# Kernel optimization log

Measured on AMD Instinct MI355X. Metric: run time of the kernel, lower is better.

Reference implementation:

```python
import jax, jax.numpy as jnp
import numpy as np

B, T, D = 4, 2048, 2048
K, D_B, TOPK, WINDOW = 7, 128, 16, 64
GATE_CAP = 1.0
STRAND_CAP = 1.0
_PHI = 1.618033988749895
_PSI = -0.6180339887498949


def _ln(x, g, b, eps=1e-5):
    m = jnp.mean(x, axis=-1, keepdims=True)
    v = jnp.mean((x - m) ** 2, axis=-1, keepdims=True)
    return (x - m) * jax.lax.rsqrt(v + eps) * g + b


def setup_inputs() -> dict:
    ks = jax.random.split(jax.random.key(0), 20)
    rn = lambda k, s, sc=1.0: jax.random.normal(k, s, jnp.float32) * sc
    d_s = 1.0 / np.sqrt(D)
    db_s = 1.0 / np.sqrt(D_B)
    return {
        'X_write': rn(ks[0], (B, T, D)),
        'X_read': rn(ks[1], (B, T, D)),
        'slots': rn(ks[2], (B, K, D_B)),
        'W0': rn(ks[3], (D, D), d_s),
        'ln_write_g': jnp.ones((D,), jnp.float32),
        'ln_write_b': jnp.zeros((D,), jnp.float32),
        'Wv': rn(ks[4], (D_B, D), d_s),
        'Wk': rn(ks[5], (D_B, D_B), db_s),
        'slot_key_bias': rn(ks[6], (K, D_B), 2.0),
        'Wg_w': rn(ks[7], (D_B, 2 * D_B), 1.0 / np.sqrt(2 * D_B)),
        'Wg_b': jnp.full((D_B,), -2.0, jnp.float32),
        'ln_strand_g': jnp.ones((D_B,), jnp.float32),
        'ln_strand_b': jnp.zeros((D_B,), jnp.float32),
        'Wsq': rn(ks[8], (D_B, D_B), db_s),
        'Wsk': rn(ks[9], (D_B, D_B), db_s),
        'Wsv': rn(ks[10], (D_B, D_B), db_s),
        'lambda_strand': rn(ks[11], (D_B,), 0.1),
        'Wq_read': rn(ks[12], (D_B, D), d_s),
        'Wk_read': rn(ks[13], (D_B, D_B), db_s),
        'Wv_read': rn(ks[14], (D, D_B), db_s),
        'render_coeffs': rn(ks[15], (K, 3, D), 0.1),
        'slot_temps': 1.0 + rn(ks[16], (K,), 0.1),
    }


def reference(X_write, X_read, slots, W0, ln_write_g, ln_write_b, Wv, Wk,
              slot_key_bias, Wg_w, Wg_b, ln_strand_g, ln_strand_b,
              Wsq, Wsk, Wsv, lambda_strand, Wq_read, Wk_read, Wv_read,
              render_coeffs, slot_temps):
    b, t, d = X_write.shape
    sd = 1.0 / np.sqrt(D_B)
    X_n = _ln(X_write, ln_write_g, ln_write_b)

    # --- banded salience + topk (torch.no_grad region; only int indices escape) ---
    W_eff = min(WINDOW, t - 1)
    Xs = jax.lax.stop_gradient(X_n)
    X_W0 = Xs @ jax.lax.stop_gradient(W0).T            # [b,t,d]
    Xp = jnp.pad(X_W0, ((0, 0), (W_eff, 0), (0, 0)))   # left-pad so offset w -> j = i + w - W

    def band_dot(w):
        return jnp.einsum('btd,btd->bt', Xs,
                          jax.lax.dynamic_slice_in_dim(Xp, w, t, axis=1))

    band = jax.vmap(band_dot)(jnp.arange(W_eff)).transpose(1, 2, 0)  # [b,t,W]
    ii = jnp.arange(t)[:, None]
    ww = jnp.arange(W_eff)[None, :]
    jj = ii + ww - W_eff
    valid = (jj >= 0) & (ii >= 1)                      # j in [max(0,i-W), i)
    sal = jnp.where(valid, band, -jnp.inf).reshape(b, -1)
    topk_eff = min(TOPK, t * (t - 1) // 2)
    _, idx = jax.lax.top_k(sal, topk_eff)              # [b,topk]
    i_idx = idx // W_eff
    j_idx = i_idx + (idx % W_eff) - W_eff

    # --- topk pair gather + bilinear relation ---
    x_new = jnp.take_along_axis(X_n, i_idx[..., None], axis=1)  # [b,topk,d]
    x_old = jnp.take_along_axis(X_n, j_idx[..., None], axis=1)
    pair_sal = jnp.sum(x_new * (x_old @ jax.lax.stop_gradient(W0).T), axis=-1)
    alpha = jax.nn.softmax(pair_sal, axis=-1)
    R_t = jnp.einsum('bp,bpe->be', alpha, (x_new - x_old) @ Wv.T)  # [b,d_b]

    # --- slot write ---
    slot_keys = slots @ Wk.T + slot_key_bias[None]
    compat = jnp.einsum('bke,be->bk', slot_keys, R_t) * sd
    compat = compat * jax.nn.softplus(slot_temps)[None]
    sw = jax.nn.softmax(compat, axis=-1)
    weighted_R = sw[..., None] * R_t[:, None, :]                 # [b,K,d_b]
    g = jax.nn.sigmoid(jnp.concatenate([slots, weighted_R], -1) @ Wg_w.T + Wg_b)
    slots_upd = (1.0 - g) * slots + g * weighted_R

    # --- strand mixer (KxK self-attention) ---
    B_ln = _ln(slots_upd, ln_strand_g, ln_strand_b)
    att = jax.nn.softmax(jnp.einsum('bke,bme->bkm', B_ln @ Wsq.T, B_ln @ Wsk.T) * sd, axis=-1)
    ctx = att @ (B_ln @ Wsv.T)
    slots_next = slots_upd + ctx * jnp.clip(jnp.tanh(lambda_strand), -STRAND_CAP, STRAND_CAP)

    # --- aux losses ---
    L_persist = jnp.mean((slots_next - slots) ** 2)
    nrm = jnp.linalg.norm(slots_next, axis=-1, keepdims=True)
    Bn = slots_next / jnp.maximum(nrm, 1e-12)
    cos = jnp.einsum('bke,bme->bkm', Bn, Bn)
    off = 1.0 - jnp.eye(K, dtype=cos.dtype)
    L_div = jnp.sum(cos ** 2 * off) / (b * K * (K - 1))

    # --- directional render gate + read ---
    q_r = X_read @ Wq_read.T                    # [b,t,d_b]
    k_r = slots_next @ Wk_read.T                # [b,K,d_b]
    v_r = slots_next @ Wv_read.T                # [b,K,d]
    scores = jnp.einsum('bte,bke->btk', q_r, k_r) * sd
    q_mean = jnp.mean(X_read, axis=1)           # [b,d]
    w0q = q_mean @ jax.lax.stop_gradient(W0).T
    dphi = _PHI - _PSI
    phi_q = (w0q - _PSI * q_mean) / dphi
    psi_q = (_PHI * q_mean - w0q) / dphi
    pm = jnp.linalg.norm(phi_q, axis=-1, keepdims=True)
    sm = jnp.linalg.norm(psi_q, axis=-1, keepdims=True)
    tot = pm + sm + 1e-6
    basis = jnp.concatenate([jnp.ones_like(pm), pm / tot, sm / tot], axis=-1)  # [b,3]
    gate = jnp.clip(jnp.tanh(jnp.einsum('bi,kid->bkd', basis, render_coeffs)),
                    -GATE_CAP, GATE_CAP)
    z = jnp.einsum('btk,bkd->btd', jax.nn.softmax(scores, axis=-1), v_r * gate)
    return z, slots_next, L_persist, L_div
```

## Files before the change

### kernel.cpp

```cpp
#include <hip/hip_runtime.h>
#include <cstdint>
#include <cstddef>

#define DEV __device__ __forceinline__

typedef __bf16 bf16x8 __attribute__((ext_vector_type(8)));
typedef float f32x4 __attribute__((ext_vector_type(4)));
typedef unsigned short u16;
typedef unsigned int u32;

constexpr int Bq = 4, Tq = 2048, Dq = 2048, Kq = 7, DB = 128, TK = 16;
constexpr float SD = 0.08838834764831845f;
constexpr float PHIc = 1.618033988749895f;
constexpr float PSIc = -0.6180339887498949f;
constexpr float DPHI = 2.2360679774997896f;
#define NEG_INF (-__builtin_inff())

DEV u16 f2bf(float f) {
  union { float f; u32 u; } x; x.f = f;
  u32 r = (x.u + 0x7fffu + ((x.u >> 16) & 1u)) >> 16;
  return (u16)r;
}
DEV float bfbits2f(u32 h) { union { u32 u; float f; } x; x.u = h << 16; return x.f; }

DEV void async16(void* l, const void* g) {
  __builtin_amdgcn_global_load_lds((const __attribute__((address_space(1))) void*)g,
                                   (__attribute__((address_space(3))) void*)l, 16, 0, 0);
}

__global__ __launch_bounds__(256) void k_prep(const float* __restrict__ W0, u16* __restrict__ W0b,
                                              const float* __restrict__ Xw, const float* __restrict__ g,
                                              const float* __restrict__ bb, u16* __restrict__ Xn,
                                              const float* __restrict__ Xr, float* __restrict__ part) {
  int bid = blockIdx.x;
  int tid = threadIdx.x;
  if (bid < 2048) {
    size_t i = ((size_t)bid * 256 + tid) * 8;
    float4 a = *(const float4*)&W0[i];
    float4 c = *(const float4*)&W0[i + 4];
    u32 p0 = (u32)f2bf(a.x) | ((u32)f2bf(a.y) << 16);
    u32 p1 = (u32)f2bf(a.z) | ((u32)f2bf(a.w) << 16);
    u32 p2 = (u32)f2bf(c.x) | ((u32)f2bf(c.y) << 16);
    u32 p3 = (u32)f2bf(c.z) | ((u32)f2bf(c.w) << 16);
    uint4 st; st.x = p0; st.y = p1; st.z = p2; st.w = p3;
    *(uint4*)&W0b[i] = st;
  } else if (bid < 2048 + 8192) {
    int row = bid - 2048;
    const float* xr = Xw + (size_t)row * Dq;
    int lane = tid & 63, w = tid >> 6;
    float4 a = *(const float4*)&xr[tid * 8];
    float4 c = *(const float4*)&xr[tid * 8 + 4];
    float s = a.x + a.y + a.z + a.w + c.x + c.y + c.z + c.w;
    float q = a.x*a.x + a.y*a.y + a.z*a.z + a.w*a.w + c.x*c.x + c.y*c.y + c.z*c.z + c.w*c.w;
    #pragma unroll
    for (int o = 32; o; o >>= 1) { s += __shfl_xor(s, o); q += __shfl_xor(q, o); }
    __shared__ float red[8];
    if (lane == 0) { red[w] = s; red[w + 4] = q; }
    __syncthreads();
    float S = red[0] + red[1] + red[2] + red[3];
    float Q = red[4] + red[5] + red[6] + red[7];
    float mean = S * (1.0f / Dq);
    float var = Q * (1.0f / Dq) - mean * mean;
    float rstd = rsqrtf(var + 1e-5f);
    float v[8] = {a.x, a.y, a.z, a.w, c.x, c.y, c.z, c.w};
    u32 p[4];
    #pragma unroll
    for (int j = 0; j < 4; ++j) {
      int d0 = tid * 8 + j * 2;
      float o0 = (v[j*2]   - mean) * rstd * g[d0]   + bb[d0];
      float o1 = (v[j*2+1] - mean) * rstd * g[d0+1] + bb[d0+1];
      p[j] = (u32)f2bf(o0) | ((u32)f2bf(o1) << 16);
    }
    uint4 st; st.x = p[0]; st.y = p[1]; st.z = p[2]; st.w = p[3];
    *(uint4*)&Xn[(size_t)row * Dq + tid * 8] = st;
  } else {
    int f = bid - (2048 + 8192);
    int s = f & 1, y = (f >> 1) & 31, b = f >> 6;
    const float* xb = Xr + (size_t)b * Tq * Dq + (size_t)s * 1024 + tid * 4;
    f32x4 acc = {0.f, 0.f, 0.f, 0.f};
    #pragma unroll 4
    for (int t = 0; t < 64; ++t) {
      const float4 v = *(const float4*)&xb[(size_t)(y * 64 + t) * Dq];
      acc[0] += v.x; acc[1] += v.y; acc[2] += v.z; acc[3] += v.w;
    }
    float4 st; st.x = acc[0]; st.y = acc[1]; st.z = acc[2]; st.w = acc[3];
    *(float4*)&part[((size_t)(b * 32 + y)) * Dq + s * 1024 + tid * 4] = st;
  }
}

__global__ __launch_bounds__(256) void k_gemm(const u16* __restrict__ A, const u16* __restrict__ B,
                                              u16* __restrict__ C, int M, int N, int K,
                                              const float* __restrict__ part, float* __restrict__ qm) {
  __shared__ u16 As[128 * 64], Bs[128 * 64];
  int tid = threadIdx.x;
  if (blockIdx.y == 16) {
    int bm = blockIdx.x;
    if (bm >= 8) return;
    int s = bm & 1, b = bm >> 1;
    int col = s * 1024 + tid * 4;
    f32x4 acc = {0.f, 0.f, 0.f, 0.f};
    #pragma unroll 8
    for (int y = 0; y < 32; ++y) {
      float4 v = *(const float4*)&part[((size_t)(b * 32 + y)) * Dq + col];
      acc[0] += v.x; acc[1] += v.y; acc[2] += v.z; acc[3] += v.w;
    }
    float4 st;
    st.x = acc[0] * (1.0f / Tq); st.y = acc[1] * (1.0f / Tq);
    st.z = acc[2] * (1.0f / Tq); st.w = acc[3] * (1.0f / Tq);
    *(float4*)&qm[(size_t)b * Dq + col] = st;
    return;
  }
  int lane = tid & 63, w = tid >> 6, wr = w >> 1, wc = w & 1;
  int bm = blockIdx.x, bn = blockIdx.y;
  const u16* Ab = A + (size_t)bm * 128 * K;
  const u16* Bb = B + (size_t)bn * 128 * K;
  f32x4 zero = {0.f, 0.f, 0.f, 0.f};
  f32x4 acc[4][4];
  #pragma unroll
  for (int mi = 0; mi < 4; ++mi)
    #pragma unroll
    for (int ni = 0; ni < 4; ++ni) acc[mi][ni] = zero;
  int ro = tid >> 3;
  int co = (tid & 7) * 8;
  int cs = co ^ ((ro & 7) * 8);
  for (int k0 = 0; k0 < K; k0 += 64) {
    #pragma unroll
    for (int i = 0; i < 4; ++i) {
      int row = ro + i * 32;
      async16(&As[row * 64 + co], Ab + (size_t)row * K + k0 + cs);
      async16(&Bs[row * 64 + co], Bb + (size_t)row * K + k0 + cs);
    }
    __syncthreads();
    #pragma unroll
    for (int ks = 0; ks < 2; ++ks) {
      int cbase = ks * 32 + ((lane >> 4) * 8);
      int crd = cbase ^ ((lane & 7) * 8);
      bf16x8 af[4], bfr[4];
      #pragma unroll
      for (int mi = 0; mi < 4; ++mi)
        af[mi] = *(const bf16x8*)&As[(wr * 64 + mi * 16 + (lane & 15)) * 64 + crd];
      #pragma unroll
      for (int ni = 0; ni < 4; ++ni)
        bfr[ni] = *(const bf16x8*)&Bs[(wc * 64 + ni * 16 + (lane & 15)) * 64 + crd];
      #pragma unroll
      for (int mi = 0; mi < 4; ++mi)
        #pragma unroll
        for (int ni = 0; ni < 4; ++ni)
          acc[mi][ni] = __builtin_amdgcn_mfma_f32_16x16x32_bf16(af[mi], bfr[ni], acc[mi][ni], 0, 0, 0);
    }
    __syncthreads();
  }
  int r0 = bm * 128 + wr * 64, c0 = bn * 128 + wc * 64;
  #pragma unroll
  for (int mi = 0; mi < 4; ++mi)
    #pragma unroll
    for (int ni = 0; ni < 4; ++ni) {
      int col = c0 + ni * 16 + (lane & 15);
      int rb = r0 + mi * 16 + ((lane >> 4) * 4);
      #pragma unroll
      for (int rg = 0; rg < 4; ++rg)
        C[(size_t)(rb + rg) * N + col] = f2bf(acc[mi][ni][rg]);
    }
}

__global__ __launch_bounds__(768) void k_band(const u16* __restrict__ Xn, const u16* __restrict__ XW0,
                                              float* __restrict__ sal,
                                              const float* __restrict__ W0, const float* __restrict__ qm,
                                              float* __restrict__ w0q) {
  int tid = threadIdx.x, lane = tid & 63, w = tid >> 6;
  if (blockIdx.y == Bq) {
    int x = blockIdx.x;
    for (int r = w; r < 32; r += 12) {
      int d = x * 32 + r;
      const float* wr = W0 + (size_t)d * Dq;
      float a0 = 0, a1 = 0, a2 = 0, a3 = 0;
      for (int e = lane * 4; e < Dq; e += 256) {
        float4 wv = *(const float4*)&wr[e];
        float4 q0 = *(const float4*)&qm[0 * Dq + e];
        float4 q1 = *(const float4*)&qm[1 * Dq + e];
        float4 q2 = *(const float4*)&qm[2 * Dq + e];
        float4 q3 = *(const float4*)&qm[3 * Dq + e];
        a0 += wv.x*q0.x + wv.y*q0.y + wv.z*q0.z + wv.w*q0.w;
        a1 += wv.x*q1.x + wv.y*q1.y + wv.z*q1.z + wv.w*q1.w;
        a2 += wv.x*q2.x + wv.y*q2.y + wv.z*q2.z + wv.w*q2.w;
        a3 += wv.x*q3.x + wv.y*q3.y + wv.z*q3.z + wv.w*q3.w;
      }
      #pragma unroll
      for (int o = 32; o; o >>= 1) {
        a0 += __shfl_xor(a0, o); a1 += __shfl_xor(a1, o);
        a2 += __shfl_xor(a2, o); a3 += __shfl_xor(a3, o);
      }
      if (lane == 0) {
        w0q[0 * Dq + d] = a0; w0q[1 * Dq + d] = a1;
        w0q[2 * Dq + d] = a2; w0q[3 * Dq + d] = a3;
      }
    }
    return;
  }
  int b = blockIdx.y, i0 = blockIdx.x * 32;
  int mi = w / 6, ni = w % 6;
  const u16* Xb = Xn + (size_t)b * Tq * Dq;
  const u16* Wb = XW0 + (size_t)b * Tq * Dq;
  int koff = (lane >> 4) * 8;
  const u16* ap = Xb + (size_t)(i0 + mi * 16 + (lane & 15)) * Dq + koff;
  int j = i0 - 64 + ni * 16 + (lane & 15); j = min(max(j, 0), Tq - 1);
  const u16* bp = Wb + (size_t)j * Dq + koff;
  f32x4 zero = {0.f, 0.f, 0.f, 0.f};
  f32x4 accA = zero, accB = zero;
  for (int k = 0; k < Dq; k += 64) {
    bf16x8 a0 = *(const bf16x8*)(ap + k);
    bf16x8 b0 = *(const bf16x8*)(bp + k);
    bf16x8 a1 = *(const bf16x8*)(ap + k + 32);
    bf16x8 b1 = *(const bf16x8*)(bp + k + 32);
    accA = __builtin_amdgcn_mfma_f32_16x16x32_bf16(a0, b0, accA, 0, 0, 0);
    accB = __builtin_amdgcn_mfma_f32_16x16x32_bf16(a1, b1, accB, 0, 0, 0);
  }
  int nl = ni * 16 + (lane & 15);
  #pragma unroll
  for (int rg = 0; rg < 4; ++rg) {
    int i = i0 + mi * 16 + (lane >> 4) * 4 + rg;
    int wb = nl - (i - i0);
    if (wb >= 0 && wb < 64) {
      int jj = i0 - 64 + nl;
      bool valid = (jj >= 0) && (i >= 1);
      sal[((size_t)b * Tq + i) * 64 + wb] = valid ? (accA[rg] + accB[rg]) : NEG_INF;
    }
  }
}

__global__ __launch_bounds__(256) void k_topk1(const float* __restrict__ sal,
                                               float* __restrict__ cv, int* __restrict__ ci,
                                               const float* __restrict__ qm, const float* __restrict__ w0q,
                                               float* __restrict__ basis) {
  int b = blockIdx.y, tid = threadIdx.x, lane = tid & 63;
  if (blockIdx.x == 128) {
    __shared__ float red[256];
    __shared__ float psum;
    float ps = 0, ss = 0;
    for (int d = tid; d < Dq; d += 256) {
      float qv = qm[b * Dq + d], wv = w0q[b * Dq + d];
      float ph = (wv - PSIc * qv) * (1.0f / DPHI);
      float pv = (PHIc * qv - wv) * (1.0f / DPHI);
      ps += ph * ph; ss += pv * pv;
    }
    red[tid] = ps; __syncthreads();
    for (int st = 128; st; st >>= 1) { if (tid < st) red[tid] += red[tid + st]; __syncthreads(); }
    if (tid == 0) psum = red[0];
    __syncthreads();
    red[tid] = ss; __syncthreads();
    for (int st = 128; st; st >>= 1) { if (tid < st) red[tid] += red[tid + st]; __syncthreads(); }
    if (tid == 0) {
      float pm = sqrtf(psum), sm = sqrtf(red[0]);
      float tot = pm + sm + 1e-6f;
      basis[b * 3 + 0] = 1.0f; basis[b * 3 + 1] = pm / tot; basis[b * 3 + 2] = sm / tot;
    }
    return;
  }
  int chunk = blockIdx.x;
  const float* s = sal + (size_t)b * Tq * 64 + (size_t)chunk * 1024;
  float lv[4]; int li[4];
  #pragma unroll
  for (int i = 0; i < 4; ++i) { lv[i] = NEG_INF; li[i] = -1; }
  #pragma unroll
  for (int i = 0; i < 4; ++i) {
    int e = tid + i * 256;
    float v = s[e];
    int idx = chunk * 1024 + e;
    if (v > lv[3]) {
      lv[3] = v; li[3] = idx;
      #pragma unroll
      for (int q = 3; q > 0; --q)
        if (lv[q] > lv[q - 1]) {
          float tv = lv[q]; lv[q] = lv[q - 1]; lv[q - 1] = tv;
          int t2 = li[q]; li[q] = li[q - 1]; li[q - 1] = t2;
        }
    }
  }
  __shared__ float Sv[256][4];
  __shared__ int Si[256][4];
  __shared__ int heads[256];
  #pragma unroll
  for (int i = 0; i < 4; ++i) { Sv[tid][i] = lv[i]; Si[tid][i] = li[i]; }
  heads[tid] = 0;
  __syncthreads();
  float* ov = cv + ((size_t)b * 128 + chunk) * 16;
  int* oi = ci + ((size_t)b * 128 + chunk) * 16;
  for (int r = 0; r < 16; ++r) {
    if (tid < 64) {
      float best = NEG_INF; int bl = 0; int bidx = 0x7fffffff;
      #pragma unroll
      for (int cc = 0; cc < 4; ++cc) {
        int c = lane + cc * 64;
        int h = heads[c];
        float v = (h < 4) ? Sv[c][h] : NEG_INF;
        int ix = (h < 4) ? Si[c][h] : 0x7fffffff;
        if (v > best || (v == best && ix < bidx)) { best = v; bl = c; bidx = ix; }
      }
      #pragma unroll
      for (int o = 32; o; o >>= 1) {
        float bv = __shfl_xor(best, o); int blx = __shfl_xor(bl, o); int bix = __shfl_xor(bidx, o);
        if (bv > best || (bv == best && bix < bidx)) { best = bv; bl = blx; bidx = bix; }
      }
      if (lane == 0) {
        int h = heads[bl];
        ov[r] = best; oi[r] = (h < 4) ? Si[bl][h] : -1;
        heads[bl] = h + 1;
      }
    }
    __syncthreads();
  }
}

__global__ __launch_bounds__(256) void k_topk2(const float* __restrict__ cv, const int* __restrict__ ci,
                                               int* __restrict__ ti, int* __restrict__ tj) {
  int b = blockIdx.x, tid = threadIdx.x, lane = tid & 63;
  __shared__ float Sv[128][16];
  __shared__ int Si[128][16];
  __shared__ int heads[128];
  __shared__ int ridx[16];
  for (int i = tid; i < 128 * 16; i += 256) {
    ((float*)Sv)[i] = cv[(size_t)b * 2048 + i];
    ((int*)Si)[i] = ci[(size_t)b * 2048 + i];
  }
  if (tid < 128) heads[tid] = 0;
  __syncthreads();
  for (int r = 0; r < 16; ++r) {
    if (tid < 64) {
      float best = NEG_INF; int bl = 0; int bidx = 0x7fffffff;
      #pragma unroll
      for (int cc = 0; cc < 2; ++cc) {
        int c = lane + cc * 64;
        int h = heads[c];
        float v = (h < 16) ? Sv[c][h] : NEG_INF;
        int ix = (h < 16) ? Si[c][h] : 0x7fffffff;
        if (v > best || (v == best && ix < bidx)) { best = v; bl = c; bidx = ix; }
      }
      #pragma unroll
      for (int o = 32; o; o >>= 1) {
        float bv = __shfl_xor(best, o); int blx = __shfl_xor(bl, o); int bix = __shfl_xor(bidx, o);
        if (bv > best || (bv == best && bix < bidx)) { best = bv; bl = blx; bidx = bix; }
      }
      if (lane == 0) {
        int h = heads[bl];
        ridx[r] = Si[bl][h];
        heads[bl] = h + 1;
      }
    }
    __syncthreads();
  }
  if (tid < 16) {
    int fi = ridx[tid];
    int ii = fi >> 6;
    int jj = ii + (fi & 63) - 64;
    ti[b * TK + tid] = ii;
    tj[b * TK + tid] = jj;
  }
}

__global__ __launch_bounds__(256) void k_gatherln(const float* __restrict__ X, const float* __restrict__ g,
    const float* __restrict__ bb, const int* __restrict__ ti, const int* __restrict__ tj,
    float* __restrict__ Xnew, float* __restrict__ Xold, float* __restrict__ psal) {
  int b = blockIdx.y, p = blockIdx.x >> 1, side = blockIdx.x & 1;
  int tid = threadIdx.x, lane = tid & 63, w = tid >> 6;
  if (blockIdx.x == 0 && tid < TK) psal[b * TK + tid] = 0.f;
  int row = side ? tj[b * TK + p] : ti[b * TK + p];
  row = min(max(row, 0), Tq - 1);
  const float* xr = X + ((size_t)(b * Tq + row)) * Dq;
  float* dst = (side ? Xold : Xnew) + ((size_t)(b * TK + p)) * Dq;
  float4 a = *(const float4*)&xr[tid * 8];
  float4 c = *(const float4*)&xr[tid * 8 + 4];
  float s = a.x + a.y + a.z + a.w + c.x + c.y + c.z + c.w;
  float q = a.x*a.x + a.y*a.y + a.z*a.z + a.w*a.w + c.x*c.x + c.y*c.y + c.z*c.z + c.w*c.w;
  #pragma unroll
  for (int o = 32; o; o >>= 1) { s += __shfl_xor(s, o); q += __shfl_xor(q, o); }
  __shared__ float red[8];
  if (lane == 0) { red[w] = s; red[w + 4] = q; }
  __syncthreads();
  float S = red[0] + red[1] + red[2] + red[3];
  float Q = red[4] + red[5] + red[6] + red[7];
  float mean = S * (1.0f / Dq);
  float var = Q * (1.0f / Dq) - mean * mean;
  float rstd = rsqrtf(var + 1e-5f);
  float v[8] = {a.x, a.y, a.z, a.w, c.x, c.y, c.z, c.w};
  float o8[8];
  #pragma unroll
  for (int j = 0; j < 8; ++j) {
    int d = tid * 8 + j;
    o8[j] = (v[j] - mean) * rstd * g[d] + bb[d];
  }
  float4 s0; s0.x = o8[0]; s0.y = o8[1]; s0.z = o8[2]; s0.w = o8[3];
  float4 s1; s1.x = o8[4]; s1.y = o8[5]; s1.z = o8[6]; s1.w = o8[7];
  *(float4*)&dst[tid * 8] = s0;
  *(float4*)&dst[tid * 8 + 4] = s1;
}

__global__ __launch_bounds__(256) void k_pairsal(const float* __restrict__ W0, const float* __restrict__ Xnew,
                                                 const float* __restrict__ Xold, float* __restrict__ psal) {
  int d0 = blockIdx.x * 64, e0 = blockIdx.y * 64;
  int tid = threadIdx.x, P = tid & 63, dg = tid >> 6;
  f32x4 xo[16];
  #pragma unroll
  for (int i = 0; i < 16; ++i)
    xo[i] = *(const f32x4*)&Xold[(size_t)P * Dq + e0 + i * 4];
  int dbase = d0 + dg * 16;
  f32x4 xn[4];
  #pragma unroll
  for (int i = 0; i < 4; ++i)
    xn[i] = *(const f32x4*)&Xnew[(size_t)P * Dq + dbase + i * 4];
  float acc = 0.f;
  #pragma unroll
  for (int dd = 0; dd < 16; ++dd) {
    int d = __builtin_amdgcn_readfirstlane(dbase + dd);
    const float* wr = W0 + (size_t)d * Dq + e0;
    float i0 = 0.f, i1 = 0.f, i2 = 0.f, i3 = 0.f;
    #pragma unroll
    for (int i = 0; i < 16; ++i) {
      float4 wv = *(const float4*)&wr[i * 4];
      i0 += wv.x * xo[i][0]; i1 += wv.y * xo[i][1];
      i2 += wv.z * xo[i][2]; i3 += wv.w * xo[i][3];
    }
    acc += xn[dd >> 2][dd & 3] * ((i0 + i1) + (i2 + i3));
  }
  __shared__ float part[4][64];
  part[dg][P] = acc;
  __syncthreads();
  if (tid < 64)
    atomicAdd(&psal[tid], part[0][tid] + part[1][tid] + part[2][tid] + part[3][tid]);
}

__global__ __launch_bounds__(256) void k_alphart(const float* __restrict__ psal, const float* __restrict__ Xnew,
    const float* __restrict__ Xold, const float* __restrict__ Wv, float* __restrict__ Rt) {
  int bx = blockIdx.x, b = blockIdx.y;
  int tid = threadIdx.x, lane = tid & 63, w = tid >> 6;
  __shared__ float al[16], xd[Dq];
  if (tid == 0) {
    float mx = NEG_INF;
    #pragma unroll
    for (int p = 0; p < 16; ++p) mx = fmaxf(mx, psal[b * 16 + p]);
    float ee[16]; float s = 0.f;
    #pragma unroll
    for (int p = 0; p < 16; ++p) { ee[p] = expf(psal[b * 16 + p] - mx); s += ee[p]; }
    #pragma unroll
    for (int p = 0; p < 16; ++p) al[p] = ee[p] / s;
  }
  __syncthreads();
  {
    int d0 = tid * 8;
    float a8[8] = {0, 0, 0, 0, 0, 0, 0, 0};
    #pragma unroll
    for (int p = 0; p < 16; ++p) {
      const float* xn = Xnew + (size_t)(b * 16 + p) * Dq + d0;
      const float* xo = Xold + (size_t)(b * 16 + p) * Dq + d0;
      float ap = al[p];
      float4 n0 = *(const float4*)xn;
      float4 n1 = *(const float4*)(xn + 4);
      float4 o0 = *(const float4*)xo;
      float4 o1 = *(const float4*)(xo + 4);
      a8[0] += ap * (n0.x - o0.x); a8[1] += ap * (n0.y - o0.y);
      a8[2] += ap * (n0.z - o0.z); a8[3] += ap * (n0.w - o0.w);
      a8[4] += ap * (n1.x - o1.x); a8[5] += ap * (n1.y - o1.y);
      a8[6] += ap * (n1.z - o1.z); a8[7] += ap * (n1.w - o1.w);
    }
    #pragma unroll
    for (int j = 0; j < 8; ++j) xd[d0 + j] = a8[j];
  }
  __syncthreads();
  int e = bx * 4 + w;
  const float* wr = Wv + (size_t)e * Dq;
  float s = 0.f;
  #pragma unroll 8
  for (int d = lane; d < Dq; d += 64) s += wr[d] * xd[d];
  #pragma unroll
  for (int o = 32; o; o >>= 1) s += __shfl_xor(s, o);
  if (lane == 0) Rt[b * DB + e] = s;
}

__global__ __launch_bounds__(256) void ksl_a(const float* __restrict__ slots, const float* __restrict__ Wk,
    const float* __restrict__ skb, const float* __restrict__ Rt, const float* __restrict__ temps,
    float* __restrict__ compat) {
  int k = blockIdx.x, b = blockIdx.y;
  int tid = threadIdx.x, g = tid >> 4, sub = tid & 15;
  __shared__ float s_s[DB], r_s[DB], sk_s[DB];
  if (tid < DB) { s_s[tid] = slots[((size_t)(b * Kq + k)) * DB + tid]; r_s[tid] = Rt[b * DB + tid]; }
  __syncthreads();
  #pragma unroll
  for (int r = 0; r < 8; ++r) {
    int e = g * 8 + r;
    const float* wr = Wk + e * DB;
    float a = 0.f;
    #pragma unroll
    for (int j = 0; j < 8; ++j) a += wr[sub + j * 16] * s_s[sub + j * 16];
    a += __shfl_xor(a, 8); a += __shfl_xor(a, 4); a += __shfl_xor(a, 2); a += __shfl_xor(a, 1);
    if (sub == 0) sk_s[e] = a + skb[k * DB + e];
  }
  __syncthreads();
  if (tid < 64) {
    float a = sk_s[tid] * r_s[tid] + sk_s[tid + 64] * r_s[tid + 64];
    #pragma unroll
    for (int o = 32; o; o >>= 1) a += __shfl_xor(a, o);
    if (tid == 0) {
      float t = temps[k];
      compat[b * Kq + k] = a * SD * log1pf(expf(t));
    }
  }
}

__global__ __launch_bounds__(256) void ksl_c(const float* __restrict__ slots, const float* __restrict__ Rt,
    const float* __restrict__ compat, const float* __restrict__ Wgw, const float* __restrict__ Wgb,
    const float* __restrict__ lng, const float* __restrict__ lnb,
    const float* __restrict__ Wsq, const float* __restrict__ Wsk, const float* __restrict__ Wsv,
    float* __restrict__ suOut, float* __restrict__ qqOut, float* __restrict__ kkOut,
    float* __restrict__ vvOut) {
  int k = blockIdx.x, b = blockIdx.y;
  int tid = threadIdx.x, g = tid >> 4, sub = tid & 15;
  __shared__ float s_s[DB], r_s[DB], su[DB], bnl[DB];
  __shared__ float mvm, mvr;
  if (tid < DB) { s_s[tid] = slots[((size_t)(b * Kq + k)) * DB + tid]; r_s[tid] = Rt[b * DB + tid]; }
  __syncthreads();
  float swk;
  {
    float cm[Kq]; float mx = NEG_INF;
    #pragma unroll
    for (int kk = 0; kk < Kq; ++kk) { cm[kk] = compat[b * Kq + kk]; mx = fmaxf(mx, cm[kk]); }
    float ssum = 0.f;
    #pragma unroll
    for (int kk = 0; kk < Kq; ++kk) { cm[kk] = expf(cm[kk] - mx); ssum += cm[kk]; }
    swk = cm[k] / ssum;
  }
  #pragma unroll
  for (int r = 0; r < 8; ++r) {
    int e = g * 8 + r;
    const float* wr = Wgw + e * 256;
    float a = 0.f;
    #pragma unroll
    for (int j = 0; j < 16; ++j) {
      int col = sub + j * 16;
      float x = (j < 8) ? s_s[col] : swk * r_s[col - 128];
      a += wr[col] * x;
    }
    a += __shfl_xor(a, 8); a += __shfl_xor(a, 4); a += __shfl_xor(a, 2); a += __shfl_xor(a, 1);
    if (sub == 0) {
      a += Wgb[e];
      float gv = 1.0f / (1.0f + expf(-a));
      float wrv = swk * r_s[e];
      su[e] = (1.0f - gv) * s_s[e] + gv * wrv;
    }
  }
  __syncthreads();
  if (tid < 64) {
    float v0 = su[tid], v1 = su[tid + 64];
    float s = v0 + v1, q = v0 * v0 + v1 * v1;
    #pragma unroll
    for (int o = 32; o; o >>= 1) { s += __shfl_xor(s, o); q += __shfl_xor(q, o); }
    if (tid == 0) {
      float m = s / DB; float va = q / DB - m * m;
      mvm = m; mvr = rsqrtf(va + 1e-5f);
    }
  }
  __syncthreads();
  if (tid < DB) {
    bnl[tid] = (su[tid] - mvm) * mvr * lng[tid] + lnb[tid];
    suOut[((size_t)(b * Kq + k)) * DB + tid] = su[tid];
  }
  __syncthreads();
  #pragma unroll
  for (int r = 0; r < 8; ++r) {
    int e = g * 8 + r;
    const float* wr1 = Wsq + e * DB;
    const float* wr2 = Wsk + e * DB;
    const float* wr3 = Wsv + e * DB;
    float a1 = 0.f, a2 = 0.f, a3 = 0.f;
    #pragma unroll
    for (int j = 0; j < 8; ++j) {
      float x = bnl[sub + j * 16];
      a1 += wr1[sub + j * 16] * x;
      a2 += wr2[sub + j * 16] * x;
      a3 += wr3[sub + j * 16] * x;
    }
    #pragma unroll
    for (int o = 8; o; o >>= 1) {
      a1 += __shfl_xor(a1, o); a2 += __shfl_xor(a2, o); a3 += __shfl_xor(a3, o);
    }
    if (sub == 0) {
      size_t oi = ((size_t)(b * Kq + k)) * DB + e;
      qqOut[oi] = a1; kkOut[oi] = a2; vvOut[oi] = a3;
    }
  }
}

__global__ __launch_bounds__(256) void ksl_d(const float* __restrict__ suOut, const float* __restrict__ qqOut,
    const float* __restrict__ kkOut, const float* __restrict__ vvOut, const float* __restrict__ lam,
    const float* __restrict__ Wkr, float* __restrict__ snOut, float* __restrict__ krOut) {
  int k = blockIdx.x, b = blockIdx.y;
  int tid = threadIdx.x, g = tid >> 4, sub = tid & 15;
  __shared__ float qq[DB], kks[Kq][DB], vvs[Kq][DB], att[8], sn_s[DB];
  if (tid < DB) qq[tid] = qqOut[((size_t)(b * Kq + k)) * DB + tid];
  for (int i = tid; i < Kq * DB; i += 256) {
    ((float*)kks)[i] = kkOut[(size_t)b * Kq * DB + i];
    ((float*)vvs)[i] = vvOut[(size_t)b * Kq * DB + i];
  }
  __syncthreads();
  if (tid < 112) {
    int m = g;
    float a = 0.f;
    #pragma unroll
    for (int j = 0; j < 8; ++j) a += qq[sub + j * 16] * kks[m][sub + j * 16];
    a += __shfl_xor(a, 8); a += __shfl_xor(a, 4); a += __shfl_xor(a, 2); a += __shfl_xor(a, 1);
    if (sub == 0) att[m] = a * SD;
  }
  __syncthreads();
  if (tid == 0) {
    float mx = att[0];
    for (int m = 1; m < Kq; ++m) mx = fmaxf(mx, att[m]);
    float s = 0.f;
    for (int m = 0; m < Kq; ++m) { att[m] = expf(att[m] - mx); s += att[m]; }
    for (int m = 0; m < Kq; ++m) att[m] /= s;
  }
  __syncthreads();
  if (tid < DB) {
    float c = 0.f;
    #pragma unroll
    for (int m = 0; m < Kq; ++m) c += att[m] * vvs[m][tid];
    float l = tanhf(lam[tid]); l = fminf(fmaxf(l, -1.0f), 1.0f);
    float v = suOut[((size_t)(b * Kq + k)) * DB + tid] + c * l;
    sn_s[tid] = v;
    snOut[((size_t)(b * Kq + k)) * DB + tid] = v;
  }
  __syncthreads();
  #pragma unroll
  for (int r = 0; r < 8; ++r) {
    int e = g * 8 + r;
    const float* wr = Wkr + e * DB;
    float a = 0.f;
    #pragma unroll
    for (int j = 0; j < 8; ++j) a += wr[sub + j * 16] * sn_s[sub + j * 16];
    a += __shfl_xor(a, 8); a += __shfl_xor(a, 4); a += __shfl_xor(a, 2); a += __shfl_xor(a, 1);
    if (sub == 0) krOut[((size_t)(b * Kq + k)) * DB + e] = a;
  }
}

__global__ __launch_bounds__(256) void k_mvg(const float* __restrict__ snOut, const float* __restrict__ krOut,
    const float* __restrict__ Wqr, const float* __restrict__ Wvr, const float* __restrict__ rc,
    const float* __restrict__ basis, const float* __restrict__ slots,
    u16* __restrict__ Mb, u16* __restrict__ Vgb, float* __restrict__ out2) {
  int b = blockIdx.y, tid = threadIdx.x;
  if (blockIdx.x == 8) {
    if (b != 0) return;
    __shared__ float red[256];
    __shared__ float nrm[28];
    float p = 0.f;
    for (int i = tid; i < Bq * Kq * DB; i += 256) { float d = snOut[i] - slots[i]; p += d * d; }
    red[tid] = p; __syncthreads();
    for (int st = 128; st; st >>= 1) { if (tid < st) red[tid] += red[tid + st]; __syncthreads(); }
    if (tid == 0) out2[0] = red[0] / (float)(Bq * Kq * DB);
    if (tid < 28) {
      int bb2 = tid / 7, k = tid % 7;
      float s = 0.f;
      for (int e = 0; e < DB; ++e) { float v = snOut[(size_t)(bb2 * 7 + k) * DB + e]; s += v * v; }
      nrm[tid] = fmaxf(sqrtf(s), 1e-12f);
    }
    __syncthreads();
    float dv = 0.f;
    if (tid < 168) {
      int bb2 = tid / 42, r = tid % 42;
      int k = r / 6, m = r % 6; m += (m >= k);
      float dot = 0.f;
      for (int e = 0; e < DB; ++e)
        dot += snOut[(size_t)(bb2 * 7 + k) * DB + e] * snOut[(size_t)(bb2 * 7 + m) * DB + e];
      float c = dot / (nrm[bb2 * 7 + k] * nrm[bb2 * 7 + m]);
      dv = c * c;
    }
    red[tid] = dv; __syncthreads();
    for (int st = 128; st; st >>= 1) { if (tid < st) red[tid] += red[tid + st]; __syncthreads(); }
    if (tid == 0) out2[1] = red[0] / 168.0f;
    return;
  }
  int d = blockIdx.x * 256 + tid;
  __shared__ float krs[Kq][DB], sns[Kq][DB];
  for (int i = tid; i < Kq * DB; i += 256) {
    ((float*)krs)[i] = krOut[(size_t)b * Kq * DB + i];
    ((float*)sns)[i] = snOut[(size_t)b * Kq * DB + i];
  }
  __syncthreads();
  float b0 = basis[b * 3 + 0], b1 = basis[b * 3 + 1], b2 = basis[b * 3 + 2];
  float am[7] = {0, 0, 0, 0, 0, 0, 0};
  for (int e = 0; e < DB; ++e) {
    float wq = Wqr[(size_t)e * Dq + d];
    #pragma unroll
    for (int k = 0; k < 7; ++k) am[k] += krs[k][e] * wq;
  }
  float vr[7] = {0, 0, 0, 0, 0, 0, 0};
  const float* wvrow = Wvr + (size_t)d * DB;
  for (int e = 0; e < DB; ++e) {
    float wv = wvrow[e];
    #pragma unroll
    for (int k = 0; k < 7; ++k) vr[k] += sns[k][e] * wv;
  }
  #pragma unroll
  for (int k = 0; k < 7; ++k) {
    Mb[((size_t)b * 7 + k) * Dq + d] = f2bf(am[k]);
    float gt = tanhf(b0 * rc[((size_t)k * 3 + 0) * Dq + d] +
                     b1 * rc[((size_t)k * 3 + 1) * Dq + d] +
                     b2 * rc[((size_t)k * 3 + 2) * Dq + d]);
    gt = fminf(fmaxf(gt, -1.0f), 1.0f);
    Vgb[((size_t)b * 7 + k) * Dq + d] = f2bf(vr[k] * gt);
  }
}

__global__ __launch_bounds__(256) void k_z(const float* __restrict__ X, const u16* __restrict__ Mb,
                                           const u16* __restrict__ Vgb, float* __restrict__ Z) {
  int b = blockIdx.y, t0 = blockIdx.x * 16;
  int tid = threadIdx.x, lane = tid & 63, w = tid >> 6;
  const u16* Ms = Mb + (size_t)b * 7 * 2048;
  const u16* Vs = Vgb + (size_t)b * 7 * 2048;
  for (int ri = 0; ri < 4; ++ri) {
    int t = t0 + ri * 4 + w;
    const float* xr = X + ((size_t)b * Tq + t) * Dq;
    float sc[7] = {0, 0, 0, 0, 0, 0, 0};
    #pragma unroll
    for (int i = 0; i < 8; ++i) {
      int d = lane * 4 + i * 256;
      float4 x = *(const float4*)&xr[d];
      #pragma unroll
      for (int k = 0; k < 7; ++k) {
        uint2 mm = *(const uint2*)&Ms[k * 2048 + d];
        sc[k] += x.x * bfbits2f(mm.x & 0xffffu) + x.y * bfbits2f(mm.x >> 16)
               + x.z * bfbits2f(mm.y & 0xffffu) + x.w * bfbits2f(mm.y >> 16);
      }
    }
    #pragma unroll
    for (int k = 0; k < 7; ++k) {
      #pragma unroll
      for (int o = 32; o; o >>= 1) sc[k] += __shfl_xor(sc[k], o);
    }
    float mx = sc[0];
    #pragma unroll
    for (int k = 1; k < 7; ++k) mx = fmaxf(mx, sc[k]);
    float pz[7]; float s = 0.f;
    #pragma unroll
    for (int k = 0; k < 7; ++k) { pz[k] = expf((sc[k] - mx) * SD); s += pz[k]; }
    float inv = 1.0f / s;
    #pragma unroll
    for (int k = 0; k < 7; ++k) pz[k] *= inv;
    float* zr = Z + ((size_t)b * Tq + t) * Dq;
    #pragma unroll
    for (int i = 0; i < 8; ++i) {
      int d = lane * 4 + i * 256;
      float4 o4; o4.x = o4.y = o4.z = o4.w = 0.f;
      #pragma unroll
      for (int k = 0; k < 7; ++k) {
        uint2 vm = *(const uint2*)&Vs[k * 2048 + d];
        float pk = pz[k];
        o4.x += pk * bfbits2f(vm.x & 0xffffu); o4.y += pk * bfbits2f(vm.x >> 16);
        o4.z += pk * bfbits2f(vm.y & 0xffffu); o4.w += pk * bfbits2f(vm.y >> 16);
      }
      *(float4*)&zr[d] = o4;
    }
  }
}

extern "C" void kernel_launch(void* const* d_in, const int* in_sizes, int n_in,
                              void* d_out, int out_size, void* d_ws, size_t ws_size,
                              hipStream_t stream) {
  const float* Xw   = (const float*)d_in[0];
  const float* Xr   = (const float*)d_in[1];
  const float* slots= (const float*)d_in[2];
  const float* W0   = (const float*)d_in[3];
  const float* lng  = (const float*)d_in[4];
  const float* lnb  = (const float*)d_in[5];
  const float* Wv   = (const float*)d_in[6];
  const float* Wk   = (const float*)d_in[7];
  const float* skb  = (const float*)d_in[8];
  const float* Wgw  = (const float*)d_in[9];
  const float* Wgb  = (const float*)d_in[10];
  const float* lsg  = (const float*)d_in[11];
  const float* lsb  = (const float*)d_in[12];
  const float* Wsq  = (const float*)d_in[13];
  const float* Wsk  = (const float*)d_in[14];
  const float* Wsv  = (const float*)d_in[15];
  const float* lam  = (const float*)d_in[16];
  const float* Wqr  = (const float*)d_in[17];
  const float* Wkr  = (const float*)d_in[18];
  const float* Wvr  = (const float*)d_in[19];
  const float* rc   = (const float*)d_in[20];
  const float* temps= (const float*)d_in[21];

  char* wsb = (char*)d_ws;
  size_t off = 0;
  auto alloc = [&](size_t bytes) -> void* {
    void* p = wsb + off;
    off += (bytes + 255) & ~(size_t)255;
    return p;
  };
  u16*   Xn   = (u16*)  alloc((size_t)Bq * Tq * Dq * 2);
  u16*   XW0  = (u16*)  alloc((size_t)Bq * Tq * Dq * 2);
  u16*   W0b  = (u16*)  alloc((size_t)Dq * Dq * 2);
  float* sal  = (float*)alloc((size_t)Bq * Tq * 64 * 4);
  int*   ti   = (int*)  alloc(Bq * TK * 4);
  int*   tj   = (int*)  alloc(Bq * TK * 4);
  float* Xnew = (float*)alloc((size_t)Bq * TK * Dq * 4);
  float* Xold = (float*)alloc((size_t)Bq * TK * Dq * 4);
  float* psal = (float*)alloc(Bq * TK * 4);
  float* Rt   = (float*)alloc(Bq * DB * 4);
  float* qm   = (float*)alloc(Bq * Dq * 4);
  float* w0q  = (float*)alloc(Bq * Dq * 4);
  float* basis= (float*)alloc(Bq * 3 * 4);
  float* krOut= (float*)alloc(Bq * Kq * DB * 4);
  u16*   Mbf  = (u16*)  alloc((size_t)Bq * Kq * Dq * 2);
  u16*   Vgb  = (u16*)  alloc((size_t)Bq * Kq * Dq * 2);
  float* cv   = (float*)alloc((size_t)Bq * 128 * 16 * 4);
  int*   ci   = (int*)  alloc((size_t)Bq * 128 * 16 * 4);
  float* part = (float*)alloc((size_t)Bq * 32 * Dq * 4);
  float* compat = (float*)alloc(Bq * Kq * 4);
  float* suB  = (float*)alloc(Bq * Kq * DB * 4);
  float* qqB  = (float*)alloc(Bq * Kq * DB * 4);
  float* kkB  = (float*)alloc(Bq * Kq * DB * 4);
  float* vvB  = (float*)alloc(Bq * Kq * DB * 4);

  float* Zout = (float*)d_out;
  float* snOut = Zout + (size_t)Bq * Tq * Dq;
  float* lossOut = snOut + Bq * Kq * DB;

  k_prep  <<<2048 + 8192 + 256, 256, 0, stream>>>(W0, W0b, Xw, lng, lnb, Xn, Xr, part);
  k_gemm  <<<dim3(64, 17), 256, 0, stream>>>(Xn, W0b, XW0, Bq * Tq, Dq, Dq, part, qm);
  k_band  <<<dim3(64, Bq + 1), 768, 0, stream>>>(Xn, XW0, sal, W0, qm, w0q);
  k_topk1 <<<dim3(129, Bq), 256, 0, stream>>>(sal, cv, ci, qm, w0q, basis);
  k_topk2 <<<Bq, 256, 0, stream>>>(cv, ci, ti, tj);
  k_gatherln<<<dim3(32, Bq), 256, 0, stream>>>(Xw, lng, lnb, ti, tj, Xnew, Xold, psal);
  k_pairsal<<<dim3(32, 32), 256, 0, stream>>>(W0, Xnew, Xold, psal);
  k_alphart<<<dim3(32, Bq), 256, 0, stream>>>(psal, Xnew, Xold, Wv, Rt);
  ksl_a   <<<dim3(Kq, Bq), 256, 0, stream>>>(slots, Wk, skb, Rt, temps, compat);
  ksl_c   <<<dim3(Kq, Bq), 256, 0, stream>>>(slots, Rt, compat, Wgw, Wgb, lsg, lsb,
                                             Wsq, Wsk, Wsv, suB, qqB, kkB, vvB);
  ksl_d   <<<dim3(Kq, Bq), 256, 0, stream>>>(suB, qqB, kkB, vvB, lam, Wkr, snOut, krOut);
  k_mvg   <<<dim3(9, Bq), 256, 0, stream>>>(snOut, krOut, Wqr, Wvr, rc, basis, slots,
                                            Mbf, Vgb, lossOut);
  k_z     <<<dim3(128, Bq), 256, 0, stream>>>(Xr, Mbf, Vgb, Zout);
}
```

Measured before the change: 400.4 us.

## Fuse per-block top-16 selection into banded salience kernel, drop salience buffer

The banded salience kernel now stages its 32x64 salience tile in shared memory and runs the first top-16 reduction in place, writing per-block candidates straight to cv/ci. The separate first top-k kernel and the global salience buffer go away, and the basis-norm work moves into the second top-k kernel as extra blocks. This removes a launch and a global round trip of the salience array. In exchange, k_band uses more shared memory and gains serial tail work (16 rounds of barrier-separated reduction) after its MFMA loop.

```diff
diff --git a/kernel.cpp b/kernel.cpp
--- a/kernel.cpp
+++ b/kernel.cpp
@@ -164,9 +164,9 @@
 }
 
 __global__ __launch_bounds__(768) void k_band(const u16* __restrict__ Xn, const u16* __restrict__ XW0,
-                                              float* __restrict__ sal,
                                               const float* __restrict__ W0, const float* __restrict__ qm,
-                                              float* __restrict__ w0q) {
+                                              float* __restrict__ w0q,
+                                              float* __restrict__ cv, int* __restrict__ ci) {
   int tid = threadIdx.x, lane = tid & 63, w = tid >> 6;
   if (blockIdx.y == Bq) {
     int x = blockIdx.x;
@@ -215,25 +215,83 @@
     accA = __builtin_amdgcn_mfma_f32_16x16x32_bf16(a0, b0, accA, 0, 0, 0);
     accB = __builtin_amdgcn_mfma_f32_16x16x32_bf16(a1, b1, accB, 0, 0, 0);
   }
+  __shared__ float sal_s[32][64];
+  __shared__ float Sv[512][4];
+  __shared__ int Si[512][4];
+  __shared__ int heads[512];
+  for (int i = tid; i < 32 * 64; i += 768) ((float*)sal_s)[i] = NEG_INF;
+  __syncthreads();
   int nl = ni * 16 + (lane & 15);
   #pragma unroll
   for (int rg = 0; rg < 4; ++rg) {
-    int i = i0 + mi * 16 + (lane >> 4) * 4 + rg;
-    int wb = nl - (i - i0);
+    int li = mi * 16 + (lane >> 4) * 4 + rg;
+    int wb = nl - li;
     if (wb >= 0 && wb < 64) {
       int jj = i0 - 64 + nl;
-      bool valid = (jj >= 0) && (i >= 1);
-      sal[((size_t)b * Tq + i) * 64 + wb] = valid ? (accA[rg] + accB[rg]) : NEG_INF;
-    }
-  }
-}
-
-__global__ __launch_bounds__(256) void k_topk1(const float* __restrict__ sal,
-                                               float* __restrict__ cv, int* __restrict__ ci,
+      bool valid = (jj >= 0) && (i0 + li >= 1);
+      sal_s[li][wb] = valid ? (accA[rg] + accB[rg]) : NEG_INF;
+    }
+  }
+  __syncthreads();
+  if (tid < 512) {
+    float lv[4]; int li_[4];
+    #pragma unroll
+    for (int i = 0; i < 4; ++i) { lv[i] = NEG_INF; li_[i] = -1; }
+    #pragma unroll
+    for (int i = 0; i < 4; ++i) {
+      int e = tid + i * 512;
+      float v = ((float*)sal_s)[e];
+      int idx = i0 * 64 + e;
+      if (v > lv[3]) {
+        lv[3] = v; li_[3] = idx;
+        #pragma unroll
+        for (int q = 3; q > 0; --q)
+          if (lv[q] > lv[q - 1]) {
+            float tv = lv[q]; lv[q] = lv[q - 1]; lv[q - 1] = tv;
+            int t2 = li_[q]; li_[q] = li_[q - 1]; li_[q - 1] = t2;
+          }
+      }
+    }
+    #pragma unroll
+    for (int i = 0; i < 4; ++i) { Sv[tid][i] = lv[i]; Si[tid][i] = li_[i]; }
+    heads[tid] = 0;
+  }
+  __syncthreads();
+  float* ov = cv + ((size_t)b * 64 + blockIdx.x) * 16;
+  int* oi = ci + ((size_t)b * 64 + blockIdx.x) * 16;
+  for (int r = 0; r < 16; ++r) {
+    if (tid < 64) {
+      float best = NEG_INF; int bl = 0; int bidx = 0x7fffffff;
+      #pragma unroll
+      for (int cc = 0; cc < 8; ++cc) {
+        int c = tid + cc * 64;
+        int h = heads[c];
+        float v = (h < 4) ? Sv[c][h] : NEG_INF;
+        int ix = (h < 4) ? Si[c][h] : 0x7fffffff;
+        if (v > best || (v == best && ix < bidx)) { best = v; bl = c; bidx = ix; }
+      }
+      #pragma unroll
+      for (int o = 32; o; o >>= 1) {
+        float bv = __shfl_xor(best, o); int blx = __shfl_xor(bl, o); int bix = __shfl_xor(bidx, o);
+        if (bv > best || (bv == best && bix < bidx)) { best = bv; bl = blx; bidx = bix; }
+      }
+      if (tid == 0) {
+        int h = heads[bl];
+        ov[r] = best; oi[r] = (h < 4) ? Si[bl][h] : -1;
+        heads[bl] = h + 1;
+      }
+    }
+    __syncthreads();
+  }
+}
+
+__global__ __launch_bounds__(256) void k_topk2(const float* __restrict__ cv, const int* __restrict__ ci,
+                                               int* __restrict__ ti, int* __restrict__ tj,
                                                const float* __restrict__ qm, const float* __restrict__ w0q,
                                                float* __restrict__ basis) {
-  int b = blockIdx.y, tid = threadIdx.x, lane = tid & 63;
-  if (blockIdx.x == 128) {
+  int tid = threadIdx.x;
+  if (blockIdx.x >= Bq) {
+    int b = blockIdx.x - Bq;
     __shared__ float red[256];
     __shared__ float psum;
     float ps = 0, ss = 0;
@@ -256,94 +314,32 @@
     }
     return;
   }
-  int chunk = blockIdx.x;
-  const float* s = sal + (size_t)b * Tq * 64 + (size_t)chunk * 1024;
-  float lv[4]; int li[4];
-  #pragma unroll
-  for (int i = 0; i < 4; ++i) { lv[i] = NEG_INF; li[i] = -1; }
-  #pragma unroll
-  for (int i = 0; i < 4; ++i) {
-    int e = tid + i * 256;
-    float v = s[e];
-    int idx = chunk * 1024 + e;
-    if (v > lv[3]) {
-      lv[3] = v; li[3] = idx;
-      #pragma unroll
-      for (int q = 3; q > 0; --q)
-        if (lv[q] > lv[q - 1]) {
-          float tv = lv[q]; lv[q] = lv[q - 1]; lv[q - 1] = tv;
-          int t2 = li[q]; li[q] = li[q - 1]; li[q - 1] = t2;
-        }
-    }
-  }
-  __shared__ float Sv[256][4];
-  __shared__ int Si[256][4];
-  __shared__ int heads[256];
-  #pragma unroll
-  for (int i = 0; i < 4; ++i) { Sv[tid][i] = lv[i]; Si[tid][i] = li[i]; }
-  heads[tid] = 0;
-  __syncthreads();
-  float* ov = cv + ((size_t)b * 128 + chunk) * 16;
-  int* oi = ci + ((size_t)b * 128 + chunk) * 16;
+  int b = blockIdx.x;
+  __shared__ float Sv[64][16];
+  __shared__ int Si[64][16];
+  __shared__ int heads[64];
+  __shared__ int ridx[16];
+  for (int i = tid; i < 64 * 16; i += 256) {
+    ((float*)Sv)[i] = cv[(size_t)b * 1024 + i];
+    ((int*)Si)[i] = ci[(size_t)b * 1024 + i];
+  }
+  if (tid < 64) heads[tid] = 0;
+  __syncthreads();
   for (int r = 0; r < 16; ++r) {
     if (tid < 64) {
-      float best = NEG_INF; int bl = 0; int bidx = 0x7fffffff;
-      #pragma unroll
-      for (int cc = 0; cc < 4; ++cc) {
-        int c = lane + cc * 64;
-        int h = heads[c];
-        float v = (h < 4) ? Sv[c][h] : NEG_INF;
-        int ix = (h < 4) ? Si[c][h] : 0x7fffffff;
-        if (v > best || (v == best && ix < bidx)) { best = v; bl = c; bidx = ix; }
-      }
+      int h = heads[tid];
+      float best = (h < 16) ? Sv[tid][h] : NEG_INF;
+      int bidx = (h < 16) ? Si[tid][h] : 0x7fffffff;
+      int bl = tid;
       #pragma unroll
       for (int o = 32; o; o >>= 1) {
         float bv = __shfl_xor(best, o); int blx = __shfl_xor(bl, o); int bix = __shfl_xor(bidx, o);
         if (bv > best || (bv == best && bix < bidx)) { best = bv; bl = blx; bidx = bix; }
       }
-      if (lane == 0) {
-        int h = heads[bl];
-        ov[r] = best; oi[r] = (h < 4) ? Si[bl][h] : -1;
-        heads[bl] = h + 1;
-      }
-    }
-    __syncthreads();
-  }
-}
-
-__global__ __launch_bounds__(256) void k_topk2(const float* __restrict__ cv, const int* __restrict__ ci,
-                                               int* __restrict__ ti, int* __restrict__ tj) {
-  int b = blockIdx.x, tid = threadIdx.x, lane = tid & 63;
-  __shared__ float Sv[128][16];
-  __shared__ int Si[128][16];
-  __shared__ int heads[128];
-  __shared__ int ridx[16];
-  for (int i = tid; i < 128 * 16; i += 256) {
-    ((float*)Sv)[i] = cv[(size_t)b * 2048 + i];
-    ((int*)Si)[i] = ci[(size_t)b * 2048 + i];
-  }
-  if (tid < 128) heads[tid] = 0;
-  __syncthreads();
-  for (int r = 0; r < 16; ++r) {
-    if (tid < 64) {
-      float best = NEG_INF; int bl = 0; int bidx = 0x7fffffff;
-      #pragma unroll
-      for (int cc = 0; cc < 2; ++cc) {
-        int c = lane + cc * 64;
-        int h = heads[c];
-        float v = (h < 16) ? Sv[c][h] : NEG_INF;
-        int ix = (h < 16) ? Si[c][h] : 0x7fffffff;
-        if (v > best || (v == best && ix < bidx)) { best = v; bl = c; bidx = ix; }
-      }
-      #pragma unroll
-      for (int o = 32; o; o >>= 1) {
-        float bv = __shfl_xor(best, o); int blx = __shfl_xor(bl, o); int bix = __shfl_xor(bidx, o);
-        if (bv > best || (bv == best && bix < bidx)) { best = bv; bl = blx; bidx = bix; }
-      }
-      if (lane == 0) {
-        int h = heads[bl];
-        ridx[r] = Si[bl][h];
-        heads[bl] = h + 1;
+      if (tid == 0) {
+        int hh = heads[bl];
+        ridx[r] = Si[bl][hh];
+        heads[bl] = hh + 1;
       }
     }
     __syncthreads();
@@ -795,7 +791,6 @@
   u16*   Xn   = (u16*)  alloc((size_t)Bq * Tq * Dq * 2);
   u16*   XW0  = (u16*)  alloc((size_t)Bq * Tq * Dq * 2);
   u16*   W0b  = (u16*)  alloc((size_t)Dq * Dq * 2);
-  float* sal  = (float*)alloc((size_t)Bq * Tq * 64 * 4);
   int*   ti   = (int*)  alloc(Bq * TK * 4);
   int*   tj   = (int*)  alloc(Bq * TK * 4);
   float* Xnew = (float*)alloc((size_t)Bq * TK * Dq * 4);
@@ -808,8 +803,8 @@
   float* krOut= (float*)alloc(Bq * Kq * DB * 4);
   u16*   Mbf  = (u16*)  alloc((size_t)Bq * Kq * Dq * 2);
   u16*   Vgb  = (u16*)  alloc((size_t)Bq * Kq * Dq * 2);
-  float* cv   = (float*)alloc((size_t)Bq * 128 * 16 * 4);
-  int*   ci   = (int*)  alloc((size_t)Bq * 128 * 16 * 4);
+  float* cv   = (float*)alloc((size_t)Bq * 64 * 16 * 4);
+  int*   ci   = (int*)  alloc((size_t)Bq * 64 * 16 * 4);
   float* part = (float*)alloc((size_t)Bq * 32 * Dq * 4);
   float* compat = (float*)alloc(Bq * Kq * 4);
   float* suB  = (float*)alloc(Bq * Kq * DB * 4);
@@ -823,9 +818,8 @@
 
   k_prep  <<<2048 + 8192 + 256, 256, 0, stream>>>(W0, W0b, Xw, lng, lnb, Xn, Xr, part);
   k_gemm  <<<dim3(64, 17), 256, 0, stream>>>(Xn, W0b, XW0, Bq * Tq, Dq, Dq, part, qm);
-  k_band  <<<dim3(64, Bq + 1), 768, 0, stream>>>(Xn, XW0, sal, W0, qm, w0q);
-  k_topk1 <<<dim3(129, Bq), 256, 0, stream>>>(sal, cv, ci, qm, w0q, basis);
-  k_topk2 <<<Bq, 256, 0, stream>>>(cv, ci, ti, tj);
+  k_band  <<<dim3(64, Bq + 1), 768, 0, stream>>>(Xn, XW0, W0, qm, w0q, cv, ci);
+  k_topk2 <<<2 * Bq, 256, 0, stream>>>(cv, ci, ti, tj, qm, w0q, basis);
   k_gatherln<<<dim3(32, Bq), 256, 0, stream>>>(Xw, lng, lnb, ti, tj, Xnew, Xold, psal);
   k_pairsal<<<dim3(32, 32), 256, 0, stream>>>(W0, Xnew, Xold, psal);
   k_alphart<<<dim3(32, Bq), 256, 0, stream>>>(psal, Xnew, Xold, Wv, Rt);
```

After: 478.6 us. 19.5% more time.
